# Optimization experiments

Measured on AMD Instinct MI355X. Metric: run time of the kernel, lower is better.

Reference implementation:

```python
import jax, jax.numpy as jnp
import numpy as np

EPS = 1e-6
THETA = 10000.0


def _rmsnorm(x, w):
    v = jnp.mean(x * x, axis=-1, keepdims=True)
    return (x * jax.lax.rsqrt(v + EPS)) * w


def _rope(x, cos, sin):
    # x: [B, S, H, hd]; cos/sin: [S, hd//2]; pairs are (even, odd) interleaved
    x0 = x[..., 0::2]
    x1 = x[..., 1::2]
    c = cos[None, :, None, :]
    s = sin[None, :, None, :]
    out = jnp.stack([x0 * c - x1 * s, x0 * s + x1 * c], axis=-1)
    return out.reshape(x.shape)


def setup_inputs() -> dict:
    B, S, D, L, V, Hff = 1, 2048, 1024, 4, 32000, 2816
    std = 0.02
    key = jax.random.key(0)
    ks = jax.random.split(key, 12)
    inp = {
        "tokens": jax.random.randint(ks[0], (B, S), 0, V, dtype=jnp.int32),
        "num_heads": 16,
        "tok_emb": jax.random.normal(ks[1], (V, D), jnp.float32) * std,
        "Wq": jax.random.normal(ks[2], (L, D, D), jnp.float32) * std,
        "Wk": jax.random.normal(ks[3], (L, D, D), jnp.float32) * std,
        "Wv": jax.random.normal(ks[4], (L, D, D), jnp.float32) * std,
        "Wo": jax.random.normal(ks[5], (L, D, D), jnp.float32) * std,
        "W1": jax.random.normal(ks[6], (L, D, Hff), jnp.float32) * std,
        "W2": jax.random.normal(ks[7], (L, Hff, D), jnp.float32) * std,
        "W3": jax.random.normal(ks[8], (L, D, Hff), jnp.float32) * std,
        "attn_norm_w": jnp.ones((L, D), jnp.float32),
        "ffn_norm_w": jnp.ones((L, D), jnp.float32),
        "final_norm_w": jnp.ones((D,), jnp.float32),
        "Wout": jax.random.normal(ks[9], (D, V), jnp.float32) * std,
    }
    return inp


def reference(tokens, num_heads, tok_emb, Wq, Wk, Wv, Wo, W1, W2, W3,
              attn_norm_w, ffn_norm_w, final_norm_w, Wout):
    B, S = tokens.shape
    D = tok_emb.shape[1]
    hd = D // num_heads
    # rotary frequencies (precompute_freqs_cis)
    inv = 1.0 / (THETA ** (jnp.arange(0, hd, 2, dtype=jnp.float32) / hd))
    ang = jnp.arange(S, dtype=jnp.float32)[:, None] * inv[None, :]  # [S, hd//2]
    cos, sin = jnp.cos(ang), jnp.sin(ang)
    # causal mask [S, S]
    mask = jnp.where(jnp.arange(S)[None, :] > jnp.arange(S)[:, None],
                     -jnp.inf, 0.0).astype(jnp.float32)
    scale = 1.0 / np.sqrt(hd).astype(np.float32)

    h = tok_emb[tokens]  # [B, S, D]

    def block(h, p):
        wq, wk, wv, wo, w1, w2, w3, anw, fnw = p
        x = _rmsnorm(h, anw)
        q = (x @ wq).reshape(B, S, num_heads, hd)
        k = (x @ wk).reshape(B, S, num_heads, hd)
        v = (x @ wv).reshape(B, S, num_heads, hd)
        q = _rope(q, cos, sin)
        k = _rope(k, cos, sin)
        scores = jnp.einsum('bqhd,bkhd->bhqk', q, k) * scale + mask
        probs = jax.nn.softmax(scores.astype(jnp.float32), axis=-1)
        o = jnp.einsum('bhqk,bkhd->bqhd', probs, v).reshape(B, S, D)
        h = h + o @ wo
        x2 = _rmsnorm(h, fnw)
        h = h + (jax.nn.silu(x2 @ w1) * (x2 @ w3)) @ w2
        return h, None

    h, _ = jax.lax.scan(
        block, h, (Wq, Wk, Wv, Wo, W1, W2, W3, attn_norm_w, ffn_norm_w))
    h = _rmsnorm(h, final_norm_w)
    # targets=None branch: logits for last position only
    logits = h[:, -1:, :] @ Wout  # [B, 1, V]
    return logits
```

## Files before the change

### kernel.cpp

```cpp
#include <hip/hip_runtime.h>
#include <stdint.h>

typedef unsigned short u16;
typedef __bf16 bf16x8 __attribute__((ext_vector_type(8)));
typedef float f32x4 __attribute__((ext_vector_type(4)));

#define AS1 __attribute__((address_space(1)))
#define AS3 __attribute__((address_space(3)))

static __device__ __forceinline__ void gload16(const void* g, void* l) {
  __builtin_amdgcn_global_load_lds((const AS1 unsigned int*)g,
                                   (AS3 unsigned int*)l, 16, 0, 0);
}

static __device__ __forceinline__ u16 f2bf(float f) {
  unsigned u = __float_as_uint(f);
  u += 0x7fffu + ((u >> 16) & 1u);
  return (u16)(u >> 16);
}

union BF8 { uint4 u; bf16x8 b; };
static __device__ __forceinline__ bf16x8 ldg_bf8(const u16* p) {
  BF8 t; t.u = *(const uint4*)p; return t.b;
}

__global__ __launch_bounds__(256) void transpose_bf16(
    const float* __restrict__ in, u16* __restrict__ out, int R, int C)
{
  __shared__ float t[32][33];
  const size_t base = (size_t)blockIdx.z * R * C;
  const float* ip = in + base;
  u16* op = out + base;
  const int c0 = blockIdx.x * 32, r0 = blockIdx.y * 32;
  const int tx = threadIdx.x & 31, ty = threadIdx.x >> 5;
#pragma unroll
  for (int i = 0; i < 4; i++)
    t[ty + i * 8][tx] = ip[(size_t)(r0 + ty + i * 8) * C + (c0 + tx)];
  __syncthreads();
#pragma unroll
  for (int i = 0; i < 4; i++)
    op[(size_t)(c0 + ty + i * 8) * R + (r0 + tx)] = f2bf(t[tx][ty + i * 8]);
}

__global__ __launch_bounds__(256) void embed_k(
    const int* __restrict__ tok, const float* __restrict__ emb, float* __restrict__ h)
{
  const int s = blockIdx.x;
  const int t = tok[s];
  ((float4*)(h + (size_t)s * 1024))[threadIdx.x] =
      ((const float4*)(emb + (size_t)t * 1024))[threadIdx.x];
}

__global__ __launch_bounds__(256) void rmsnorm_bf16(
    const float* __restrict__ x, const float* __restrict__ w, u16* __restrict__ y)
{
  const int s = blockIdx.x, tid = threadIdx.x;
  const float4 v = ((const float4*)(x + (size_t)s * 1024))[tid];
  float ss = v.x * v.x + v.y * v.y + v.z * v.z + v.w * v.w;
#pragma unroll
  for (int off = 32; off; off >>= 1) ss += __shfl_xor(ss, off);
  __shared__ float red[4];
  if ((tid & 63) == 0) red[tid >> 6] = ss;
  __syncthreads();
  const float tot = red[0] + red[1] + red[2] + red[3];
  const float sc = rsqrtf(tot * (1.0f / 1024.0f) + 1e-6f);
  const float4 wv = ((const float4*)w)[tid];
  ushort4 o;
  o.x = f2bf(v.x * sc * wv.x);
  o.y = f2bf(v.y * sc * wv.y);
  o.z = f2bf(v.z * sc * wv.z);
  o.w = f2bf(v.w * sc * wv.w);
  ((ushort4*)(y + (size_t)s * 1024))[tid] = o;
}

__global__ __launch_bounds__(256) void gemm_bt(
    int M, int N, int K,
    const u16* __restrict__ A,
    const u16* __restrict__ Bz0, const u16* __restrict__ Bz1, const u16* __restrict__ Bz2,
    float* __restrict__ Cz0, float* __restrict__ Cz1, float* __restrict__ Cz2,
    int doAdd)
{
  const u16* B = (blockIdx.z == 0) ? Bz0 : (blockIdx.z == 1) ? Bz1 : Bz2;
  float*    C = (blockIdx.z == 0) ? Cz0 : (blockIdx.z == 1) ? Cz1 : Cz2;
  __shared__ u16 As[128 * 32];
  __shared__ u16 Bs[128 * 32];
  const int tid = threadIdx.x;
  const int wave = tid >> 6, lane = tid & 63;
  const int lm = lane & 15, quad = lane >> 4;
  const int wm = wave >> 1, wn = wave & 1;
  const int m0 = blockIdx.y * 128, n0 = blockIdx.x * 128;

  const int c0 = tid, c1 = tid + 256;
  const u16* ga0 = A + (size_t)(m0 + (c0 >> 2)) * K + (c0 & 3) * 8;
  const u16* ga1 = A + (size_t)(m0 + (c1 >> 2)) * K + (c1 & 3) * 8;
  const u16* gb0 = B + (size_t)(n0 + (c0 >> 2)) * K + (c0 & 3) * 8;
  const u16* gb1 = B + (size_t)(n0 + (c1 >> 2)) * K + (c1 & 3) * 8;
  u16* la0 = &As[c0 * 8];
  u16* la1 = &As[c1 * 8];
  u16* lb0 = &Bs[c0 * 8];
  u16* lb1 = &Bs[c1 * 8];

  f32x4 acc[4][4];
#pragma unroll
  for (int i = 0; i < 4; i++)
#pragma unroll
    for (int j = 0; j < 4; j++) acc[i][j] = (f32x4){0.f, 0.f, 0.f, 0.f};

  const u16* arp = &As[(wm * 64 + lm) * 32 + quad * 8];
  const u16* brp = &Bs[(wn * 64 + lm) * 32 + quad * 8];

  for (int k0 = 0; k0 < K; k0 += 32) {
    __syncthreads();
    gload16(ga0 + k0, la0);
    gload16(ga1 + k0, la1);
    gload16(gb0 + k0, lb0);
    gload16(gb1 + k0, lb1);
    __syncthreads();
    bf16x8 af[4], bfv[4];
#pragma unroll
    for (int mi = 0; mi < 4; mi++) af[mi] = *(const bf16x8*)(arp + mi * 16 * 32);
#pragma unroll
    for (int ni = 0; ni < 4; ni++) bfv[ni] = *(const bf16x8*)(brp + ni * 16 * 32);
#pragma unroll
    for (int mi = 0; mi < 4; mi++)
#pragma unroll
      for (int ni = 0; ni < 4; ni++)
        acc[mi][ni] = __builtin_amdgcn_mfma_f32_16x16x32_bf16(af[mi], bfv[ni], acc[mi][ni], 0, 0, 0);
  }

#pragma unroll
  for (int mi = 0; mi < 4; mi++) {
    const int row = m0 + wm * 64 + mi * 16 + quad * 4;
#pragma unroll
    for (int ni = 0; ni < 4; ni++) {
      const int col = n0 + wn * 64 + ni * 16 + lm;
      float* cp = C + (size_t)row * N + col;
      if (doAdd) {
#pragma unroll
        for (int r = 0; r < 4; r++) cp[(size_t)r * N] += acc[mi][ni][r];
      } else {
#pragma unroll
        for (int r = 0; r < 4; r++) cp[(size_t)r * N] = acc[mi][ni][r];
      }
    }
  }
}

__global__ __launch_bounds__(256) void gemm_bt64(
    int M, int N, int K, const u16* __restrict__ A, const u16* __restrict__ B,
    float* __restrict__ C)
{
  __shared__ u16 As[128 * 32];
  __shared__ u16 Bs[64 * 32];
  const int tid = threadIdx.x;
  const int wave = tid >> 6, lane = tid & 63;
  const int lm = lane & 15, quad = lane >> 4;
  const int m0 = blockIdx.y * 128, n0 = blockIdx.x * 64;

  const int c0 = tid, c1 = tid + 256;
  const u16* ga0 = A + (size_t)(m0 + (c0 >> 2)) * K + (c0 & 3) * 8;
  const u16* ga1 = A + (size_t)(m0 + (c1 >> 2)) * K + (c1 & 3) * 8;
  const u16* gb0 = B + (size_t)(n0 + (c0 >> 2)) * K + (c0 & 3) * 8;
  u16* la0 = &As[c0 * 8];
  u16* la1 = &As[c1 * 8];
  u16* lb0 = &Bs[c0 * 8];

  f32x4 acc[2][4];
#pragma unroll
  for (int i = 0; i < 2; i++)
#pragma unroll
    for (int j = 0; j < 4; j++) acc[i][j] = (f32x4){0.f, 0.f, 0.f, 0.f};

  const u16* arp = &As[(wave * 32 + lm) * 32 + quad * 8];
  const u16* brp = &Bs[lm * 32 + quad * 8];

  for (int k0 = 0; k0 < K; k0 += 32) {
    __syncthreads();
    gload16(ga0 + k0, la0);
    gload16(ga1 + k0, la1);
    gload16(gb0 + k0, lb0);
    __syncthreads();
    bf16x8 af[2], bfv[4];
#pragma unroll
    for (int mi = 0; mi < 2; mi++) af[mi] = *(const bf16x8*)(arp + mi * 16 * 32);
#pragma unroll
    for (int ni = 0; ni < 4; ni++) bfv[ni] = *(const bf16x8*)(brp + ni * 16 * 32);
#pragma unroll
    for (int mi = 0; mi < 2; mi++)
#pragma unroll
      for (int ni = 0; ni < 4; ni++)
        acc[mi][ni] = __builtin_amdgcn_mfma_f32_16x16x32_bf16(af[mi], bfv[ni], acc[mi][ni], 0, 0, 0);
  }

#pragma unroll
  for (int mi = 0; mi < 2; mi++) {
    const int row = m0 + wave * 32 + mi * 16 + quad * 4;
#pragma unroll
    for (int ni = 0; ni < 4; ni++) {
      const int col = n0 + ni * 16 + lm;
      float* cp = C + (size_t)row * N + col;
#pragma unroll
      for (int r = 0; r < 4; r++) cp[(size_t)r * N] += acc[mi][ni][r];
    }
  }
}

__global__ __launch_bounds__(256) void rope_qk(
    const float* __restrict__ qf, const float* __restrict__ kf,
    u16* __restrict__ qb, u16* __restrict__ kb)
{
  const int idx = blockIdx.x * 256 + threadIdx.x;
  const int s = idx >> 9;
  const int p = idx & 511;
  const int h = p >> 5, i = p & 31;
  const size_t o = (size_t)s * 1024 + h * 64 + 2 * i;
  const float freq = __expf((float)i * (-9.210340371976184f / 32.0f));
  const float ang = (float)s * freq;
  float sn, cs;
  sincosf(ang, &sn, &cs);
  const float2 q = *(const float2*)(qf + o);
  const float2 k = *(const float2*)(kf + o);
  ushort2 qo, ko;
  qo.x = f2bf(q.x * cs - q.y * sn); qo.y = f2bf(q.x * sn + q.y * cs);
  ko.x = f2bf(k.x * cs - k.y * sn); ko.y = f2bf(k.x * sn + k.y * cs);
  *(ushort2*)(qb + o) = qo;
  *(ushort2*)(kb + o) = ko;
}

struct KFr { bf16x8 b[8]; };

__global__ __launch_bounds__(256) void attn_fa(
    const u16* __restrict__ Q, const u16* __restrict__ Kb,
    const u16* __restrict__ Vt, u16* __restrict__ O)
{
  const int head = blockIdx.y;
  const int wave = threadIdx.x >> 6, lane = threadIdx.x & 63;
  const int lm = lane & 15, quad = lane >> 4;
  const int qblk = 31 - blockIdx.x;
  const int q0 = qblk * 64 + wave * 16;
  const int nc = qblk + 1;
  __shared__ __align__(16) float Pb[4][16][72];
  float (*P)[72] = Pb[wave];
  const float scale = 0.125f;

  const u16* qp = Q + (size_t)(q0 + lm) * 1024 + head * 64 + quad * 8;
  const bf16x8 aq0 = ldg_bf8(qp);
  const bf16x8 aq1 = ldg_bf8(qp + 32);

  f32x4 o[4];
#pragma unroll
  for (int i = 0; i < 4; i++) o[i] = (f32x4){0.f, 0.f, 0.f, 0.f};
  float mrun[4] = {-1e30f, -1e30f, -1e30f, -1e30f};
  float lrun[4] = {0.f, 0.f, 0.f, 0.f};

  auto loadK = [&](KFr& kr, int kc) {
    const u16* kp = Kb + (size_t)(kc + lm) * 1024 + head * 64 + quad * 8;
#pragma unroll
    for (int j = 0; j < 4; j++) {
      kr.b[j * 2 + 0] = ldg_bf8(kp + (size_t)j * 16 * 1024);
      kr.b[j * 2 + 1] = ldg_bf8(kp + (size_t)j * 16 * 1024 + 32);
    }
  };

  auto compute = [&](const KFr& kr, int kc) {
    bf16x8 vv[8];
    const u16* vp = Vt + (size_t)(head * 64 + lm) * 2048 + kc + quad * 8;
#pragma unroll
    for (int nd = 0; nd < 4; nd++) {
      vv[nd * 2 + 0] = ldg_bf8(vp + (size_t)nd * 16 * 2048);
      vv[nd * 2 + 1] = ldg_bf8(vp + (size_t)nd * 16 * 2048 + 32);
    }
    const f32x4 z = (f32x4){0.f, 0.f, 0.f, 0.f};
    f32x4 S[4];
#pragma unroll
    for (int j = 0; j < 4; j++) {
      S[j] = __builtin_amdgcn_mfma_f32_16x16x32_bf16(aq0, kr.b[j * 2 + 0], z, 0, 0, 0);
      S[j] = __builtin_amdgcn_mfma_f32_16x16x32_bf16(aq1, kr.b[j * 2 + 1], S[j], 0, 0, 0);
    }
    float p[4][4], alpha[4], mx[4], rs[4];
#pragma unroll
    for (int r = 0; r < 4; r++) {
      const int row = q0 + quad * 4 + r;
      mx[r] = -1e30f;
#pragma unroll
      for (int j = 0; j < 4; j++) {
        float s = S[j][r] * scale;
        if (kc + j * 16 + lm > row) s = -1e30f;
        p[j][r] = s;
        mx[r] = fmaxf(mx[r], s);
      }
    }
#pragma unroll
    for (int off = 1; off < 16; off <<= 1)
#pragma unroll
      for (int r = 0; r < 4; r++) mx[r] = fmaxf(mx[r], __shfl_xor(mx[r], off));
#pragma unroll
    for (int r = 0; r < 4; r++) {
      const float mnew = fmaxf(mrun[r], mx[r]);
      alpha[r] = __expf(mrun[r] - mnew);
      mrun[r] = mnew;
      rs[r] = 0.f;
#pragma unroll
      for (int j = 0; j < 4; j++) {
        p[j][r] = __expf(p[j][r] - mnew);
        rs[r] += p[j][r];
      }
    }
#pragma unroll
    for (int off = 1; off < 16; off <<= 1)
#pragma unroll
      for (int r = 0; r < 4; r++) rs[r] += __shfl_xor(rs[r], off);
#pragma unroll
    for (int r = 0; r < 4; r++) {
      lrun[r] = lrun[r] * alpha[r] + rs[r];
#pragma unroll
      for (int j = 0; j < 4; j++) P[quad * 4 + r][j * 16 + lm] = p[j][r];
      o[0][r] *= alpha[r]; o[1][r] *= alpha[r];
      o[2][r] *= alpha[r]; o[3][r] *= alpha[r];
    }
    const float* pr0 = &P[lm][quad * 8];
    const float4 pa = *(const float4*)pr0;
    const float4 pb2 = *(const float4*)(pr0 + 4);
    const float4 pc = *(const float4*)(pr0 + 32);
    const float4 pd = *(const float4*)(pr0 + 36);
    BF8 t0, t1;
    u16* s0 = (u16*)&t0; u16* s1 = (u16*)&t1;
    s0[0] = f2bf(pa.x); s0[1] = f2bf(pa.y); s0[2] = f2bf(pa.z); s0[3] = f2bf(pa.w);
    s0[4] = f2bf(pb2.x); s0[5] = f2bf(pb2.y); s0[6] = f2bf(pb2.z); s0[7] = f2bf(pb2.w);
    s1[0] = f2bf(pc.x); s1[1] = f2bf(pc.y); s1[2] = f2bf(pc.z); s1[3] = f2bf(pc.w);
    s1[4] = f2bf(pd.x); s1[5] = f2bf(pd.y); s1[6] = f2bf(pd.z); s1[7] = f2bf(pd.w);
#pragma unroll
    for (int nd = 0; nd < 4; nd++) {
      o[nd] = __builtin_amdgcn_mfma_f32_16x16x32_bf16(t0.b, vv[nd * 2 + 0], o[nd], 0, 0, 0);
      o[nd] = __builtin_amdgcn_mfma_f32_16x16x32_bf16(t1.b, vv[nd * 2 + 1], o[nd], 0, 0, 0);
    }
  };

  KFr kA, kB;
  loadK(kA, 0);
  int c = 0;
  while (true) {
    if (c + 1 < nc) loadK(kB, (c + 1) * 64);
    compute(kA, c * 64);
    if (++c == nc) break;
    if (c + 1 < nc) loadK(kA, (c + 1) * 64);
    compute(kB, c * 64);
    if (++c == nc) break;
  }

#pragma unroll
  for (int r = 0; r < 4; r++) {
    const float inv = 1.0f / lrun[r];
    const int row = q0 + quad * 4 + r;
    u16* op = O + (size_t)row * 1024 + head * 64 + lm;
#pragma unroll
    for (int nd = 0; nd < 4; nd++) op[nd * 16] = f2bf(o[nd][r] * inv);
  }
}

__global__ __launch_bounds__(256) void silu_mul(
    const float* __restrict__ g1, const float* __restrict__ g3, u16* __restrict__ u)
{
  const int idx = blockIdx.x * 256 + threadIdx.x;
  const float4 a = ((const float4*)g1)[idx];
  const float4 b = ((const float4*)g3)[idx];
  ushort4 o;
  o.x = f2bf(a.x / (1.f + __expf(-a.x)) * b.x);
  o.y = f2bf(a.y / (1.f + __expf(-a.y)) * b.y);
  o.z = f2bf(a.z / (1.f + __expf(-a.z)) * b.z);
  o.w = f2bf(a.w / (1.f + __expf(-a.w)) * b.w);
  ((ushort4*)u)[idx] = o;
}

__global__ __launch_bounds__(256) void final_norm(
    const float* __restrict__ h, const float* __restrict__ w, float* __restrict__ xn)
{
  const int tid = threadIdx.x;
  const float4 v = ((const float4*)(h + (size_t)2047 * 1024))[tid];
  float ss = v.x * v.x + v.y * v.y + v.z * v.z + v.w * v.w;
#pragma unroll
  for (int off = 32; off; off >>= 1) ss += __shfl_xor(ss, off);
  __shared__ float red[4];
  if ((tid & 63) == 0) red[tid >> 6] = ss;
  __syncthreads();
  const float tot = red[0] + red[1] + red[2] + red[3];
  const float sc = rsqrtf(tot * (1.0f / 1024.0f) + 1e-6f);
  const float4 wv = ((const float4*)w)[tid];
  float4 o;
  o.x = v.x * sc * wv.x; o.y = v.y * sc * wv.y;
  o.z = v.z * sc * wv.z; o.w = v.w * sc * wv.w;
  ((float4*)xn)[tid] = o;
}

__global__ __launch_bounds__(256) void logits_k(
    const float* __restrict__ xn, const float* __restrict__ Wout, float* __restrict__ out)
{
  const int v = blockIdx.x * 256 + threadIdx.x;
  const int dp = blockIdx.y;
  const float* xp = xn + dp * 256;
  const float* wp = Wout + (size_t)dp * 256 * 32000 + v;
  float acc = 0.f;
#pragma unroll 8
  for (int d = 0; d < 256; d++) acc = fmaf(xp[d], wp[(size_t)d * 32000], acc);
  atomicAdd(out + v, acc);
}

extern "C" void kernel_launch(void* const* d_in, const int* in_sizes, int n_in,
                              void* d_out, int out_size, void* d_ws, size_t ws_size,
                              hipStream_t stream) {
  const int S = 2048, D = 1024, HFF = 2816, L = 4;
  const int* tokens = (const int*)d_in[0];
  const float* tok_emb = (const float*)d_in[2];
  const float* Wq = (const float*)d_in[3];
  const float* Wk = (const float*)d_in[4];
  const float* Wv = (const float*)d_in[5];
  const float* Wo = (const float*)d_in[6];
  const float* W1 = (const float*)d_in[7];
  const float* W2 = (const float*)d_in[8];
  const float* W3 = (const float*)d_in[9];
  const float* anw  = (const float*)d_in[10];
  const float* fnw  = (const float*)d_in[11];
  const float* finw = (const float*)d_in[12];
  const float* Wout = (const float*)d_in[13];

  char* w = (char*)d_ws;
  size_t off = 0;
  auto take = [&](size_t b) { size_t o = off; off += (b + 255) & ~(size_t)255; return o; };
  const size_t szDD = (size_t)L * D * D * 2;
  const size_t szDH = (size_t)L * D * HFF * 2;
  u16* WqT = (u16*)(w + take(szDD));
  u16* WkT = (u16*)(w + take(szDD));
  u16* WvT = (u16*)(w + take(szDD));
  u16* WoT = (u16*)(w + take(szDD));
  u16* W1T = (u16*)(w + take(szDH));
  u16* W3T = (u16*)(w + take(szDH));
  u16* W2T = (u16*)(w + take(szDH));
  float* h  = (float*)(w + take((size_t)S * D * 4));
  u16*   xb = (u16*)(w + take((size_t)S * D * 2));
  const size_t region = take((size_t)2 * S * HFF * 4 + (size_t)S * HFF * 2);
  float* qf = (float*)(w + region);
  float* kf = qf + (size_t)S * D;
  float* vf = kf + (size_t)S * D;
  u16* qbb = (u16*)(vf + (size_t)S * D);
  u16* kbb = qbb + (size_t)S * D;
  u16* vTb = kbb + (size_t)S * D;
  u16* ob  = vTb + (size_t)S * D;
  float* g1 = (float*)(w + region);
  float* g3 = g1 + (size_t)S * HFF;
  u16*  ub  = (u16*)(g3 + (size_t)S * HFF);
  float* xn = (float*)(w + take(4096));
  (void)ws_size; (void)in_sizes; (void)n_in; (void)out_size;

  const dim3 blk(256);
  transpose_bf16<<<dim3(32, 32, 4), blk, 0, stream>>>(Wq, WqT, D, D);
  transpose_bf16<<<dim3(32, 32, 4), blk, 0, stream>>>(Wk, WkT, D, D);
  transpose_bf16<<<dim3(32, 32, 4), blk, 0, stream>>>(Wv, WvT, D, D);
  transpose_bf16<<<dim3(32, 32, 4), blk, 0, stream>>>(Wo, WoT, D, D);
  transpose_bf16<<<dim3(88, 32, 4), blk, 0, stream>>>(W1, W1T, D, HFF);
  transpose_bf16<<<dim3(88, 32, 4), blk, 0, stream>>>(W3, W3T, D, HFF);
  transpose_bf16<<<dim3(32, 88, 4), blk, 0, stream>>>(W2, W2T, HFF, D);
  embed_k<<<2048, blk, 0, stream>>>(tokens, tok_emb, h);

  for (int l = 0; l < L; l++) {
    const size_t oDD = (size_t)l * D * D;
    const size_t oDH = (size_t)l * D * HFF;
    rmsnorm_bf16<<<2048, blk, 0, stream>>>(h, anw + l * D, xb);
    gemm_bt<<<dim3(8, 16, 3), blk, 0, stream>>>(S, D, D, xb,
        WqT + oDD, WkT + oDD, WvT + oDD, qf, kf, vf, 0);
    rope_qk<<<4096, blk, 0, stream>>>(qf, kf, qbb, kbb);
    transpose_bf16<<<dim3(32, 64, 1), blk, 0, stream>>>(vf, vTb, S, D);
    attn_fa<<<dim3(32, 16), blk, 0, stream>>>(qbb, kbb, vTb, ob);
    gemm_bt64<<<dim3(16, 16), blk, 0, stream>>>(S, D, D, ob, WoT + oDD, h);
    rmsnorm_bf16<<<2048, blk, 0, stream>>>(h, fnw + l * D, xb);
    gemm_bt<<<dim3(22, 16, 2), blk, 0, stream>>>(S, HFF, D, xb,
        W1T + oDH, W3T + oDH, W3T + oDH, g1, g3, g3, 0);
    silu_mul<<<5632, blk, 0, stream>>>(g1, g3, ub);
    gemm_bt64<<<dim3(16, 16), blk, 0, stream>>>(S, D, HFF, ub, W2T + oDH, h);
  }
  final_norm<<<1, blk, 0, stream>>>(h, finw, xn);
  hipMemsetAsync(d_out, 0, 32000 * sizeof(float), stream);
  logits_k<<<dim3(125, 4), blk, 0, stream>>>(xn, Wout, (float*)d_out);
}
```

Before: 1.592 ms.

## Split causal attention along keys into four partitions with combine pass

```diff
diff --git a/kernel.cpp b/kernel.cpp
--- a/kernel.cpp
+++ b/kernel.cpp
@@ -229,16 +229,33 @@
 
 struct KFr { bf16x8 b[8]; };
 
-__global__ __launch_bounds__(256) void attn_fa(
+__global__ __launch_bounds__(256) void attn_fa_part(
     const u16* __restrict__ Q, const u16* __restrict__ Kb,
-    const u16* __restrict__ Vt, u16* __restrict__ O)
+    const u16* __restrict__ Vt,
+    u16* __restrict__ po, float* __restrict__ pm, float* __restrict__ pl)
 {
   const int head = blockIdx.y;
+  const int sp = blockIdx.z;
+  const int qblk = 31 - blockIdx.x;
+  const int nc = qblk + 1;
+  const int cb = sp * nc / 4, ce = (sp + 1) * nc / 4;
+
+  const size_t blkIdx = (size_t)((sp * 16 + head) * 32 + qblk);
+  u16*   poB = po + blkIdx * 64 * 64;
+  float* pmB = pm + blkIdx * 64;
+  float* plB = pl + blkIdx * 64;
+
+  if (cb == ce) {
+    const uint4 z4 = {0u, 0u, 0u, 0u};
+    ((uint4*)poB)[threadIdx.x] = z4;
+    ((uint4*)poB)[threadIdx.x + 256] = z4;
+    if (threadIdx.x < 64) { pmB[threadIdx.x] = -1e30f; plB[threadIdx.x] = 0.f; }
+    return;
+  }
+
   const int wave = threadIdx.x >> 6, lane = threadIdx.x & 63;
   const int lm = lane & 15, quad = lane >> 4;
-  const int qblk = 31 - blockIdx.x;
   const int q0 = qblk * 64 + wave * 16;
-  const int nc = qblk + 1;
   __shared__ __align__(16) float Pb[4][16][72];
   float (*P)[72] = Pb[wave];
   const float scale = 0.125f;
@@ -337,25 +354,70 @@
   };
 
   KFr kA, kB;
-  loadK(kA, 0);
-  int c = 0;
+  loadK(kA, cb * 64);
+  int c = cb;
   while (true) {
-    if (c + 1 < nc) loadK(kB, (c + 1) * 64);
+    if (c + 1 < ce) loadK(kB, (c + 1) * 64);
     compute(kA, c * 64);
-    if (++c == nc) break;
-    if (c + 1 < nc) loadK(kA, (c + 1) * 64);
+    if (++c == ce) break;
+    if (c + 1 < ce) loadK(kA, (c + 1) * 64);
     compute(kB, c * 64);
-    if (++c == nc) break;
+    if (++c == ce) break;
   }
 
 #pragma unroll
   for (int r = 0; r < 4; r++) {
-    const float inv = 1.0f / lrun[r];
-    const int row = q0 + quad * 4 + r;
-    u16* op = O + (size_t)row * 1024 + head * 64 + lm;
-#pragma unroll
-    for (int nd = 0; nd < 4; nd++) op[nd * 16] = f2bf(o[nd][r] * inv);
-  }
+    const int rl = wave * 16 + quad * 4 + r;
+    if (lm == 0) { pmB[rl] = mrun[r]; plB[rl] = lrun[r]; }
+    u16* op = poB + (size_t)rl * 64 + lm;
+#pragma unroll
+    for (int nd = 0; nd < 4; nd++) op[nd * 16] = f2bf(o[nd][r]);
+  }
+}
+
+__global__ __launch_bounds__(256) void attn_combine(
+    const u16* __restrict__ po, const float* __restrict__ pm,
+    const float* __restrict__ pl, u16* __restrict__ O)
+{
+  const int qblk = blockIdx.x, head = blockIdx.y;
+  const int r = threadIdx.x >> 2;
+  const int d0 = (threadIdx.x & 3) * 16;
+  const size_t idx = ((size_t)head * 32 + qblk) * 64 + r;
+  const size_t PSTR = (size_t)16 * 32 * 64;
+  float m[4], l[4], M = -1e30f;
+#pragma unroll
+  for (int s = 0; s < 4; s++) {
+    m[s] = pm[s * PSTR + idx];
+    l[s] = pl[s * PSTR + idx];
+    M = fmaxf(M, m[s]);
+  }
+  float L = 0.f, acc[16];
+#pragma unroll
+  for (int j = 0; j < 16; j++) acc[j] = 0.f;
+#pragma unroll
+  for (int s = 0; s < 4; s++) {
+    const float w = __expf(m[s] - M);
+    L += w * l[s];
+    const u16* p = po + (s * PSTR + idx) * 64 + d0;
+    const bf16x8 a = ldg_bf8(p);
+    const bf16x8 b = ldg_bf8(p + 8);
+#pragma unroll
+    for (int j = 0; j < 8; j++) {
+      acc[j]     += w * (float)a[j];
+      acc[8 + j] += w * (float)b[j];
+    }
+  }
+  const float inv = 1.f / L;
+  BF8 t0, t1;
+  u16* s0 = (u16*)&t0; u16* s1 = (u16*)&t1;
+#pragma unroll
+  for (int j = 0; j < 8; j++) {
+    s0[j] = f2bf(acc[j] * inv);
+    s1[j] = f2bf(acc[8 + j] * inv);
+  }
+  u16* op = O + (size_t)(qblk * 64 + r) * 1024 + head * 64 + d0;
+  *(uint4*)op = t0.u;
+  *(uint4*)(op + 8) = t1.u;
 }
 
 __global__ __launch_bounds__(256) void silu_mul(
@@ -448,6 +510,9 @@
   float* g1 = (float*)(w + region);
   float* g3 = g1 + (size_t)S * HFF;
   u16*  ub  = (u16*)(g3 + (size_t)S * HFF);
+  u16*   po  = (u16*)qf;
+  float* pmb = vf;
+  float* plb = vf + (size_t)4 * 16 * 32 * 64;
   float* xn = (float*)(w + take(4096));
   (void)ws_size; (void)in_sizes; (void)n_in; (void)out_size;
 
@@ -469,7 +534,8 @@
         WqT + oDD, WkT + oDD, WvT + oDD, qf, kf, vf, 0);
     rope_qk<<<4096, blk, 0, stream>>>(qf, kf, qbb, kbb);
     transpose_bf16<<<dim3(32, 64, 1), blk, 0, stream>>>(vf, vTb, S, D);
-    attn_fa<<<dim3(32, 16), blk, 0, stream>>>(qbb, kbb, vTb, ob);
+    attn_fa_part<<<dim3(32, 16, 4), blk, 0, stream>>>(qbb, kbb, vTb, po, pmb, plb);
+    attn_combine<<<dim3(32, 16), blk, 0, stream>>>(po, pmb, plb, ob);
     gemm_bt64<<<dim3(16, 16), blk, 0, stream>>>(S, D, D, ob, WoT + oDD, h);
     rmsnorm_bf16<<<2048, blk, 0, stream>>>(h, fnw + l * D, xb);
     gemm_bt<<<dim3(22, 16, 2), blk, 0, stream>>>(S, HFF, D, xb,
```

Measured after the change: 1.623 ms. No clear change (+2.0%).

## Compute transposed scores in attention to keep P in registers, drop LDS round-trip

Applied to the files above, without the earlier changes.

```diff
diff --git a/kernel.cpp b/kernel.cpp
--- a/kernel.cpp
+++ b/kernel.cpp
@@ -239,19 +239,19 @@
   const int qblk = 31 - blockIdx.x;
   const int q0 = qblk * 64 + wave * 16;
   const int nc = qblk + 1;
-  __shared__ __align__(16) float Pb[4][16][72];
-  float (*P)[72] = Pb[wave];
-  const float scale = 0.125f;
+  const float sc_l2 = 0.125f * 1.4426950408889634f;
+  const int qrow = q0 + lm;
 
   const u16* qp = Q + (size_t)(q0 + lm) * 1024 + head * 64 + quad * 8;
   const bf16x8 aq0 = ldg_bf8(qp);
   const bf16x8 aq1 = ldg_bf8(qp + 32);
+  const u16* vbase = Vt + (size_t)(head * 64 + lm) * 2048;
 
   f32x4 o[4];
 #pragma unroll
   for (int i = 0; i < 4; i++) o[i] = (f32x4){0.f, 0.f, 0.f, 0.f};
-  float mrun[4] = {-1e30f, -1e30f, -1e30f, -1e30f};
-  float lrun[4] = {0.f, 0.f, 0.f, 0.f};
+  float mrun = -1e30f;
+  float lrun = 0.f;
 
   auto loadK = [&](KFr& kr, int kc) {
     const u16* kp = Kb + (size_t)(kc + lm) * 1024 + head * 64 + quad * 8;
@@ -263,77 +263,78 @@
   };
 
   auto compute = [&](const KFr& kr, int kc) {
-    bf16x8 vv[8];
-    const u16* vp = Vt + (size_t)(head * 64 + lm) * 2048 + kc + quad * 8;
-#pragma unroll
-    for (int nd = 0; nd < 4; nd++) {
-      vv[nd * 2 + 0] = ldg_bf8(vp + (size_t)nd * 16 * 2048);
-      vv[nd * 2 + 1] = ldg_bf8(vp + (size_t)nd * 16 * 2048 + 32);
-    }
+    BF8 vv[2][4];
+#pragma unroll
+    for (int h = 0; h < 2; h++)
+#pragma unroll
+      for (int nd = 0; nd < 4; nd++) {
+        const u16* vp = vbase + (size_t)nd * 16 * 2048 + kc + h * 32 + quad * 4;
+        const uint2 lo = *(const uint2*)vp;
+        const uint2 hi = *(const uint2*)(vp + 16);
+        vv[h][nd].u = (uint4){lo.x, lo.y, hi.x, hi.y};
+      }
     const f32x4 z = (f32x4){0.f, 0.f, 0.f, 0.f};
     f32x4 S[4];
 #pragma unroll
     for (int j = 0; j < 4; j++) {
-      S[j] = __builtin_amdgcn_mfma_f32_16x16x32_bf16(aq0, kr.b[j * 2 + 0], z, 0, 0, 0);
-      S[j] = __builtin_amdgcn_mfma_f32_16x16x32_bf16(aq1, kr.b[j * 2 + 1], S[j], 0, 0, 0);
-    }
-    float p[4][4], alpha[4], mx[4], rs[4];
-#pragma unroll
-    for (int r = 0; r < 4; r++) {
-      const int row = q0 + quad * 4 + r;
-      mx[r] = -1e30f;
-#pragma unroll
-      for (int j = 0; j < 4; j++) {
-        float s = S[j][r] * scale;
-        if (kc + j * 16 + lm > row) s = -1e30f;
-        p[j][r] = s;
-        mx[r] = fmaxf(mx[r], s);
+      S[j] = __builtin_amdgcn_mfma_f32_16x16x32_bf16(kr.b[j * 2 + 0], aq0, z, 0, 0, 0);
+      S[j] = __builtin_amdgcn_mfma_f32_16x16x32_bf16(kr.b[j * 2 + 1], aq1, S[j], 0, 0, 0);
+    }
+    float p[4][4];
+#pragma unroll
+    for (int j = 0; j < 4; j++)
+#pragma unroll
+      for (int r = 0; r < 4; r++) p[j][r] = S[j][r] * sc_l2;
+    if (kc + 63 > q0) {
+#pragma unroll
+      for (int j = 0; j < 4; j++)
+#pragma unroll
+        for (int r = 0; r < 4; r++)
+          if (kc + 16 * j + 4 * quad + r > qrow) p[j][r] = -1e30f;
+    }
+    float mx = -1e30f;
+#pragma unroll
+    for (int j = 0; j < 4; j++)
+#pragma unroll
+      for (int r = 0; r < 4; r++) mx = fmaxf(mx, p[j][r]);
+    mx = fmaxf(mx, __shfl_xor(mx, 16));
+    mx = fmaxf(mx, __shfl_xor(mx, 32));
+    const float mnew = fmaxf(mrun, mx);
+    const float alpha = exp2f(mrun - mnew);
+    mrun = mnew;
+    float rs = 0.f;
+#pragma unroll
+    for (int j = 0; j < 4; j++)
+#pragma unroll
+      for (int r = 0; r < 4; r++) {
+        p[j][r] = exp2f(p[j][r] - mnew);
+        rs += p[j][r];
       }
-    }
-#pragma unroll
-    for (int off = 1; off < 16; off <<= 1)
-#pragma unroll
-      for (int r = 0; r < 4; r++) mx[r] = fmaxf(mx[r], __shfl_xor(mx[r], off));
-#pragma unroll
-    for (int r = 0; r < 4; r++) {
-      const float mnew = fmaxf(mrun[r], mx[r]);
-      alpha[r] = __expf(mrun[r] - mnew);
-      mrun[r] = mnew;
-      rs[r] = 0.f;
-#pragma unroll
-      for (int j = 0; j < 4; j++) {
-        p[j][r] = __expf(p[j][r] - mnew);
-        rs[r] += p[j][r];
+    rs += __shfl_xor(rs, 16);
+    rs += __shfl_xor(rs, 32);
+    lrun = lrun * alpha + rs;
+    float alr[4];
+#pragma unroll
+    for (int r = 0; r < 4; r++) alr[r] = __shfl(alpha, quad * 4 + r);
+#pragma unroll
+    for (int nd = 0; nd < 4; nd++)
+#pragma unroll
+      for (int r = 0; r < 4; r++) o[nd][r] *= alr[r];
+    BF8 fa[2];
+#pragma unroll
+    for (int h = 0; h < 2; h++) {
+      u16* s = (u16*)&fa[h];
+#pragma unroll
+      for (int r = 0; r < 4; r++) {
+        s[r]     = f2bf(p[2 * h][r]);
+        s[4 + r] = f2bf(p[2 * h + 1][r]);
       }
     }
 #pragma unroll
-    for (int off = 1; off < 16; off <<= 1)
-#pragma unroll
-      for (int r = 0; r < 4; r++) rs[r] += __shfl_xor(rs[r], off);
-#pragma unroll
-    for (int r = 0; r < 4; r++) {
-      lrun[r] = lrun[r] * alpha[r] + rs[r];
-#pragma unroll
-      for (int j = 0; j < 4; j++) P[quad * 4 + r][j * 16 + lm] = p[j][r];
-      o[0][r] *= alpha[r]; o[1][r] *= alpha[r];
-      o[2][r] *= alpha[r]; o[3][r] *= alpha[r];
-    }
-    const float* pr0 = &P[lm][quad * 8];
-    const float4 pa = *(const float4*)pr0;
-    const float4 pb2 = *(const float4*)(pr0 + 4);
-    const float4 pc = *(const float4*)(pr0 + 32);
-    const float4 pd = *(const float4*)(pr0 + 36);
-    BF8 t0, t1;
-    u16* s0 = (u16*)&t0; u16* s1 = (u16*)&t1;
-    s0[0] = f2bf(pa.x); s0[1] = f2bf(pa.y); s0[2] = f2bf(pa.z); s0[3] = f2bf(pa.w);
-    s0[4] = f2bf(pb2.x); s0[5] = f2bf(pb2.y); s0[6] = f2bf(pb2.z); s0[7] = f2bf(pb2.w);
-    s1[0] = f2bf(pc.x); s1[1] = f2bf(pc.y); s1[2] = f2bf(pc.z); s1[3] = f2bf(pc.w);
-    s1[4] = f2bf(pd.x); s1[5] = f2bf(pd.y); s1[6] = f2bf(pd.z); s1[7] = f2bf(pd.w);
-#pragma unroll
-    for (int nd = 0; nd < 4; nd++) {
-      o[nd] = __builtin_amdgcn_mfma_f32_16x16x32_bf16(t0.b, vv[nd * 2 + 0], o[nd], 0, 0, 0);
-      o[nd] = __builtin_amdgcn_mfma_f32_16x16x32_bf16(t1.b, vv[nd * 2 + 1], o[nd], 0, 0, 0);
-    }
+    for (int h = 0; h < 2; h++)
+#pragma unroll
+      for (int nd = 0; nd < 4; nd++)
+        o[nd] = __builtin_amdgcn_mfma_f32_16x16x32_bf16(fa[h].b, vv[h][nd].b, o[nd], 0, 0, 0);
   };
 
   KFr kA, kB;
@@ -350,11 +351,11 @@
 
 #pragma unroll
   for (int r = 0; r < 4; r++) {
-    const float inv = 1.0f / lrun[r];
+    const float linv = 1.0f / __shfl(lrun, quad * 4 + r);
     const int row = q0 + quad * 4 + r;
     u16* op = O + (size_t)row * 1024 + head * 64 + lm;
 #pragma unroll
-    for (int nd = 0; nd < 4; nd++) op[nd * 16] = f2bf(o[nd][r] * inv);
+    for (int nd = 0; nd < 4; nd++) op[nd * 16] = f2bf(o[nd][r] * linv);
   }
 }
 
```

Result: slower. 1.813 ms (+13.9%).
